# Performance work log

Hardware: AMD Instinct MI355X
Metric: run time of the kernel (lower is better)

The kernel has to match this reference:

```python
import jax, jax.numpy as jnp
import numpy as np

B, S, D = 4, 4096, 64
D_MODEL = 64


def setup_inputs() -> dict:
    key = jax.random.key(0)
    kq, kk, kv, km = jax.random.split(key, 4)
    q = jax.random.normal(kq, (B, S, D), dtype=jnp.float32)
    k = jax.random.normal(kk, (B, S, D), dtype=jnp.float32)
    v = jax.random.normal(kv, (B, S, D), dtype=jnp.float32)
    mask = jax.random.uniform(km, (B, S, S), dtype=jnp.float32)
    return {"q": q, "k": k, "v": v, "mask": mask}


def reference(q, k, v, mask):
    dk = jnp.sqrt(jnp.asarray(D_MODEL, dtype=q.dtype))
    # [B,S,S] scores; multiplicative (non-additive) mask applied pre-softmax
    scaled_qk = jnp.einsum('bqd,bkd->bqk', q, k) / dk
    scaled_qk = scaled_qk * mask
    attn = jax.nn.softmax(scaled_qk, axis=-1)
    return jnp.einsum('bqk,bkd->bqd', attn, v)
```

## Files before the change

kernel.cpp:

```cpp
#include <hip/hip_runtime.h>
#include <hip/hip_bf16.h>

#define S_LEN 4096
#define DH 64
#define NBATCH 4

typedef __attribute__((ext_vector_type(8))) short bf16x8;
typedef __attribute__((ext_vector_type(4))) short bf16x4;
typedef __attribute__((ext_vector_type(4))) float f32x4;

static __device__ __forceinline__ short f2bf(float x) {
  __hip_bfloat16 h = __float2bfloat16(x);
  return *reinterpret_cast<short*>(&h);
}

#define MFMA(a, b, c) __builtin_amdgcn_mfma_f32_16x16x32_bf16((a), (b), (c), 0, 0, 0)

__global__ __launch_bounds__(256) void cvt_q_kernel(const float* __restrict__ q,
                                                    short* __restrict__ qb) {
  int i = (blockIdx.x * 256 + threadIdx.x) * 4;
  f32x4 x = *(const f32x4*)(q + i);
  bf16x4 o;
#pragma unroll
  for (int j = 0; j < 4; ++j) o[j] = f2bf(x[j]);
  *(bf16x4*)(qb + i) = o;
}

__global__ __launch_bounds__(256) void cvt_frag_kernel(const float* __restrict__ k,
                                                       const float* __restrict__ v,
                                                       short* __restrict__ kfrag,
                                                       short* __restrict__ vfrag) {
  __shared__ short kt[32][80];
  __shared__ short vt[32][80];
  const int t = threadIdx.x;
  const int b = blockIdx.x >> 7;
  const int i = blockIdx.x & 127;
  const size_t src0 = ((size_t)b * S_LEN + i * 32) * DH;
  {
    const int row = t >> 3, c0 = (t & 7) * 8;
    const f32x4 xk0 = *(const f32x4*)(k + src0 + row * DH + c0);
    const f32x4 xk1 = *(const f32x4*)(k + src0 + row * DH + c0 + 4);
    const f32x4 xv0 = *(const f32x4*)(v + src0 + row * DH + c0);
    const f32x4 xv1 = *(const f32x4*)(v + src0 + row * DH + c0 + 4);
#pragma unroll
    for (int j = 0; j < 4; ++j) {
      kt[row][c0 + j] = f2bf(xk0[j]);  kt[row][c0 + 4 + j] = f2bf(xk1[j]);
      vt[row][c0 + j] = f2bf(xv0[j]);  vt[row][c0 + 4 + j] = f2bf(xv1[j]);
    }
  }
  __syncthreads();
  const int c = t >> 6, l = t & 63;
  const size_t dst = (((size_t)(b * 128 + i) * 4 + c) * 64 + l) * 8;
  {
    const int kr = ((c >> 1) * 16) + (l & 15);
    const int d0 = ((c & 1) * 32) + (l >> 4) * 8;
    *(bf16x8*)(kfrag + dst) = *(const bf16x8*)&kt[kr][d0];
  }
  {
    bf16x8 f;
    const int col = c * 16 + (l & 15);
    const int r0 = (l >> 4) * 8;
#pragma unroll
    for (int j = 0; j < 8; ++j) f[j] = vt[r0 + j][col];
    *(bf16x8*)(vfrag + dst) = f;
  }
}

__global__ __launch_bounds__(512, 2) void fa_kernel(
    const short* __restrict__ qb, const short* __restrict__ kfrag,
    const short* __restrict__ vfrag, const float* __restrict__ mask,
    float* __restrict__ out) {
  __shared__ __align__(16) short lds_p[8][16][40];
  __shared__ float lds_O[8][16][64];
  __shared__ float lds_l[8][16];

  const int tid = threadIdx.x;
  const int w = tid >> 6;
  const int wq = w >> 1;
  const int wk = w & 1;
  const int lane = tid & 63;
  const int quad = lane >> 4;
  const int n16 = lane & 15;
  const int loff = lane * 8;

  const int vb = ((blockIdx.x & 7) << 5) | (blockIdx.x >> 3);
  const int b = vb >> 6;
  const int q0 = (vb & 63) << 6;

  const int qr = q0 + wq * 16 + n16;
  const short* qrow = qb + (size_t)(b * S_LEN + qr) * DH;
  const bf16x8 aQ0 = *(const bf16x8*)(qrow + quad * 8);
  const bf16x8 aQ1 = *(const bf16x8*)(qrow + 32 + quad * 8);

  f32x4 O0 = {0.f, 0.f, 0.f, 0.f}, O1 = O0, O2 = O0, O3 = O0;
  float lacc = 0.f;

  const float* mrow = mask + ((size_t)b * S_LEN + qr) * S_LEN + quad * 4;
  const short* kfb = kfrag + (size_t)(b * 128 + wk) * 2048;
  const short* vfb = vfrag + (size_t)(b * 128 + wk) * 2048;

  bf16x8 kA0, kA1, kA2, kA3, kB0, kB1, kB2, kB3;
  bf16x8 vA0, vA1, vA2, vA3, vB0, vB1, vB2, vB3;
  f32x4 mA0, mA1, mB0, mB1, mC0, mC1, mD0, mD1;

#define LOAD_BK(B0, B1, B2, B3, SS)                       \
  {                                                       \
    const short* kf_ = kfb + (size_t)(SS) * 4096 + loff;  \
    B0 = *(const bf16x8*)(kf_);                           \
    B1 = *(const bf16x8*)(kf_ + 512);                     \
    B2 = *(const bf16x8*)(kf_ + 1024);                    \
    B3 = *(const bf16x8*)(kf_ + 1536);                    \
  }

#define LOAD_BV(V0, V1, V2, V3, SS)                       \
  {                                                       \
    const short* vf_ = vfb + (size_t)(SS) * 4096 + loff;  \
    V0 = *(const bf16x8*)(vf_);                           \
    V1 = *(const bf16x8*)(vf_ + 512);                     \
    V2 = *(const bf16x8*)(vf_ + 1024);                    \
    V3 = *(const bf16x8*)(vf_ + 1536);                    \
  }

#define LOAD_MASK(D0, D1, LK)                             \
  {                                                       \
    const float* mp_ = mrow + (LK);                       \
    D0 = *(const f32x4*)(mp_);                            \
    D1 = *(const f32x4*)(mp_ + 16);                       \
  }

#define FA_STEP(K0, K1, K2, K3, V0, V1, V2, V3, M0, M1, SS)                \
  {                                                                        \
    const f32x4 z = {0.f, 0.f, 0.f, 0.f};                                  \
    f32x4 s0 = MFMA(K0, aQ0, z); s0 = MFMA(K1, aQ1, s0);                   \
    f32x4 s1 = MFMA(K2, aQ0, z); s1 = MFMA(K3, aQ1, s1);                   \
    LOAD_BK(K0, K1, K2, K3, ((SS) + 2) & 63);          \
    float p0_[4], p1_[4];                                                  \
    _Pragma("unroll") for (int r = 0; r < 4; ++r) {                        \
      p0_[r] = __expf(s0[r] * 0.125f * M0[r]);                             \
      p1_[r] = __expf(s1[r] * 0.125f * M1[r]);                             \
      lacc += p0_[r] + p1_[r];                                             \
    }                                                                      \
    LOAD_MASK(M0, M1, (((SS) + 4) * 64 + wk * 32) & 4095);     \
    bf16x4 w0_, w1_;                                                       \
    _Pragma("unroll") for (int r = 0; r < 4; ++r) {                        \
      w0_[r] = f2bf(p0_[r]); w1_[r] = f2bf(p1_[r]);                        \
    }                                                                      \
    *(bf16x4*)&lds_p[w][n16][quad * 4] = w0_;                              \
    *(bf16x4*)&lds_p[w][n16][16 + quad * 4] = w1_;                         \
    const bf16x8 aP = *(const bf16x8*)&lds_p[w][n16][quad * 8];            \
    O0 = MFMA(aP, V0, O0); O1 = MFMA(aP, V1, O1);                          \
    O2 = MFMA(aP, V2, O2); O3 = MFMA(aP, V3, O3);                          \
    LOAD_BV(V0, V1, V2, V3, ((SS) + 2) & 63);          \
  }

  LOAD_BK(kA0, kA1, kA2, kA3, 0);
  LOAD_BK(kB0, kB1, kB2, kB3, 1);
  LOAD_BV(vA0, vA1, vA2, vA3, 0);
  LOAD_BV(vB0, vB1, vB2, vB3, 1);
  LOAD_MASK(mA0, mA1, wk * 32);
  LOAD_MASK(mB0, mB1, 64 + wk * 32);
  LOAD_MASK(mC0, mC1, 128 + wk * 32);
  LOAD_MASK(mD0, mD1, 192 + wk * 32);

#pragma unroll 1
  for (int it = 0; it < 16; ++it) {
    const int s4 = it * 4;
    FA_STEP(kA0, kA1, kA2, kA3, vA0, vA1, vA2, vA3, mA0, mA1, s4);
    FA_STEP(kB0, kB1, kB2, kB3, vB0, vB1, vB2, vB3, mB0, mB1, s4 + 1);
    FA_STEP(kA0, kA1, kA2, kA3, vA0, vA1, vA2, vA3, mC0, mC1, s4 + 2);
    FA_STEP(kB0, kB1, kB2, kB3, vB0, vB1, vB2, vB3, mD0, mD1, s4 + 3);
  }
#undef LOAD_BK
#undef LOAD_BV
#undef LOAD_MASK
#undef FA_STEP

  lacc += __shfl_xor(lacc, 16);
  lacc += __shfl_xor(lacc, 32);

#pragma unroll
  for (int r = 0; r < 4; ++r) {
    const int row = quad * 4 + r;
    lds_O[w][row][n16]      = O0[r];
    lds_O[w][row][16 + n16] = O1[r];
    lds_O[w][row][32 + n16] = O2[r];
    lds_O[w][row][48 + n16] = O3[r];
  }
  if (lane < 16) lds_l[w][lane] = lacc;
  __syncthreads();

  const int g = tid >> 7;
  const int r = (tid >> 3) & 15;
  const int c8 = (tid & 7) << 3;
  const int w0 = g * 2, w1 = g * 2 + 1;
  const float inv = 1.0f / (lds_l[w0][r] + lds_l[w1][r]);
  float* op = out + (size_t)(b * S_LEN + q0 + g * 16 + r) * DH + c8;
  f32x4 acc0, acc1;
#pragma unroll
  for (int j = 0; j < 4; ++j) {
    acc0[j] = (lds_O[w0][r][c8 + j]     + lds_O[w1][r][c8 + j])     * inv;
    acc1[j] = (lds_O[w0][r][c8 + 4 + j] + lds_O[w1][r][c8 + 4 + j]) * inv;
  }
  *(f32x4*)(op) = acc0;
  *(f32x4*)(op + 4) = acc1;
}

extern "C" void kernel_launch(void* const* d_in, const int* in_sizes, int n_in,
                              void* d_out, int out_size, void* d_ws, size_t ws_size,
                              hipStream_t stream) {
  const float* q = (const float*)d_in[0];
  const float* k = (const float*)d_in[1];
  const float* v = (const float*)d_in[2];
  const float* mask = (const float*)d_in[3];
  float* out = (float*)d_out;

  short* qb = (short*)d_ws;
  short* kfrag = qb + (size_t)NBATCH * S_LEN * DH;
  short* vfrag = kfrag + (size_t)NBATCH * S_LEN * DH;

  cvt_q_kernel<<<(NBATCH * S_LEN * DH) / 1024, 256, 0, stream>>>(q, qb);
  cvt_frag_kernel<<<NBATCH * 128, 256, 0, stream>>>(k, v, kfrag, vfrag);
  fa_kernel<<<NBATCH * 64, 512, 0, stream>>>(qb, kfrag, vfrag, mask, out);
}
```

Before: 402.9 us.

## Stage K/V fragments and mask tiles through double-buffered LDS

Replaces per-wave register prefetch of K/V fragments and mask values with cooperative loads by all 8 waves into double-buffered LDS, using XOR-swizzled mask slots. Each step reads the current tile from LDS and writes the next one, followed by a block-wide barrier. This removes the duplicate global loads of K/V made by waves that share the same key split, and shrinks register pressure. In exchange it adds a __syncthreads every step, LDS traffic, and a shorter prefetch distance (one step instead of two to four).

```diff
diff --git a/kernel.cpp b/kernel.cpp
--- a/kernel.cpp
+++ b/kernel.cpp
@@ -70,6 +70,9 @@
     const short* __restrict__ qb, const short* __restrict__ kfrag,
     const short* __restrict__ vfrag, const float* __restrict__ mask,
     float* __restrict__ out) {
+  __shared__ __align__(16) short kst[2][2][4][512];
+  __shared__ __align__(16) short vst[2][2][4][512];
+  __shared__ __align__(16) float mst[2][4096];
   __shared__ __align__(16) short lds_p[8][16][40];
   __shared__ float lds_O[8][16][64];
   __shared__ float lds_l[8][16];
@@ -95,52 +98,44 @@
   f32x4 O0 = {0.f, 0.f, 0.f, 0.f}, O1 = O0, O2 = O0, O3 = O0;
   float lacc = 0.f;
 
-  const float* mrow = mask + ((size_t)b * S_LEN + qr) * S_LEN + quad * 4;
-  const short* kfb = kfrag + (size_t)(b * 128 + wk) * 2048;
-  const short* vfb = vfrag + (size_t)(b * 128 + wk) * 2048;
-
-  bf16x8 kA0, kA1, kA2, kA3, kB0, kB1, kB2, kB3;
-  bf16x8 vA0, vA1, vA2, vA3, vB0, vB1, vB2, vB3;
-  f32x4 mA0, mA1, mB0, mB1, mC0, mC1, mD0, mD1;
-
-#define LOAD_BK(B0, B1, B2, B3, SS)                       \
-  {                                                       \
-    const short* kf_ = kfb + (size_t)(SS) * 4096 + loff;  \
-    B0 = *(const bf16x8*)(kf_);                           \
-    B1 = *(const bf16x8*)(kf_ + 512);                     \
-    B2 = *(const bf16x8*)(kf_ + 1024);                    \
-    B3 = *(const bf16x8*)(kf_ + 1536);                    \
-  }
-
-#define LOAD_BV(V0, V1, V2, V3, SS)                       \
-  {                                                       \
-    const short* vf_ = vfb + (size_t)(SS) * 4096 + loff;  \
-    V0 = *(const bf16x8*)(vf_);                           \
-    V1 = *(const bf16x8*)(vf_ + 512);                     \
-    V2 = *(const bf16x8*)(vf_ + 1024);                    \
-    V3 = *(const bf16x8*)(vf_ + 1536);                    \
-  }
-
-#define LOAD_MASK(D0, D1, LK)                             \
-  {                                                       \
-    const float* mp_ = mrow + (LK);                       \
-    D0 = *(const f32x4*)(mp_);                            \
-    D1 = *(const f32x4*)(mp_ + 16);                       \
-  }
-
-#define FA_STEP(K0, K1, K2, K3, V0, V1, V2, V3, M0, M1, SS)                \
+  const int ksp = w >> 2, kfr = w & 3;
+  const short* kbase =
+      kfrag + (size_t)(b * 128 + ksp) * 2048 + kfr * 512 + loff;
+  const short* vbase =
+      vfrag + (size_t)(b * 128 + ksp) * 2048 + kfr * 512 + loff;
+  const int srow0 = w * 8 + (lane >> 4);
+  const int srow1 = srow0 + 4;
+  const int sg = lane & 15;
+  const float* msrc0 =
+      mask + ((size_t)b * S_LEN + q0 + srow0) * S_LEN + sg * 4;
+  const float* msrc1 =
+      mask + ((size_t)b * S_LEN + q0 + srow1) * S_LEN + sg * 4;
+  const int wslot0 = srow0 * 64 + (sg ^ (srow0 & 7)) * 4;
+  const int wslot1 = srow1 * 64 + (sg ^ (srow1 & 7)) * 4;
+  const int mr = wq * 16 + n16;
+  const int rslot0 = mr * 64 + (((wk * 8 + quad) ^ (mr & 7)) * 4);
+  const int rslot1 = mr * 64 + (((wk * 8 + 4 + quad) ^ (mr & 7)) * 4);
+
+#define STEP(CUR, SS)                                                      \
   {                                                                        \
+    const int sn_ = ((SS) + 1) & 63; \
+    const bf16x8 kR = *(const bf16x8*)(kbase + (size_t)sn_ * 4096);        \
+    const bf16x8 vR = *(const bf16x8*)(vbase + (size_t)sn_ * 4096);        \
+    const f32x4 mR0 = *(const f32x4*)(msrc0 + sn_ * 64);                   \
+    const f32x4 mR1 = *(const f32x4*)(msrc1 + sn_ * 64);                   \
     const f32x4 z = {0.f, 0.f, 0.f, 0.f};                                  \
-    f32x4 s0 = MFMA(K0, aQ0, z); s0 = MFMA(K1, aQ1, s0);                   \
-    f32x4 s1 = MFMA(K2, aQ0, z); s1 = MFMA(K3, aQ1, s1);                   \
-    LOAD_BK(K0, K1, K2, K3, ((SS) + 2) & 63);          \
+    f32x4 s0 = MFMA(*(const bf16x8*)&kst[CUR][wk][0][loff], aQ0, z);       \
+    s0 = MFMA(*(const bf16x8*)&kst[CUR][wk][1][loff], aQ1, s0);            \
+    f32x4 s1 = MFMA(*(const bf16x8*)&kst[CUR][wk][2][loff], aQ0, z);       \
+    s1 = MFMA(*(const bf16x8*)&kst[CUR][wk][3][loff], aQ1, s1);            \
+    const f32x4 M0 = *(const f32x4*)&mst[CUR][rslot0];                     \
+    const f32x4 M1 = *(const f32x4*)&mst[CUR][rslot1];                     \
     float p0_[4], p1_[4];                                                  \
     _Pragma("unroll") for (int r = 0; r < 4; ++r) {                        \
       p0_[r] = __expf(s0[r] * 0.125f * M0[r]);                             \
       p1_[r] = __expf(s1[r] * 0.125f * M1[r]);                             \
       lacc += p0_[r] + p1_[r];                                             \
     }                                                                      \
-    LOAD_MASK(M0, M1, (((SS) + 4) * 64 + wk * 32) & 4095);     \
     bf16x4 w0_, w1_;                                                       \
     _Pragma("unroll") for (int r = 0; r < 4; ++r) {                        \
       w0_[r] = f2bf(p0_[r]); w1_[r] = f2bf(p1_[r]);                        \
@@ -148,32 +143,35 @@
     *(bf16x4*)&lds_p[w][n16][quad * 4] = w0_;                              \
     *(bf16x4*)&lds_p[w][n16][16 + quad * 4] = w1_;                         \
     const bf16x8 aP = *(const bf16x8*)&lds_p[w][n16][quad * 8];            \
-    O0 = MFMA(aP, V0, O0); O1 = MFMA(aP, V1, O1);                          \
-    O2 = MFMA(aP, V2, O2); O3 = MFMA(aP, V3, O3);                          \
-    LOAD_BV(V0, V1, V2, V3, ((SS) + 2) & 63);          \
-  }
-
-  LOAD_BK(kA0, kA1, kA2, kA3, 0);
-  LOAD_BK(kB0, kB1, kB2, kB3, 1);
-  LOAD_BV(vA0, vA1, vA2, vA3, 0);
-  LOAD_BV(vB0, vB1, vB2, vB3, 1);
-  LOAD_MASK(mA0, mA1, wk * 32);
-  LOAD_MASK(mB0, mB1, 64 + wk * 32);
-  LOAD_MASK(mC0, mC1, 128 + wk * 32);
-  LOAD_MASK(mD0, mD1, 192 + wk * 32);
+    O0 = MFMA(aP, *(const bf16x8*)&vst[CUR][wk][0][loff], O0);             \
+    O1 = MFMA(aP, *(const bf16x8*)&vst[CUR][wk][1][loff], O1);             \
+    O2 = MFMA(aP, *(const bf16x8*)&vst[CUR][wk][2][loff], O2);             \
+    O3 = MFMA(aP, *(const bf16x8*)&vst[CUR][wk][3][loff], O3);             \
+    *(bf16x8*)&kst[(CUR) ^ 1][ksp][kfr][loff] = kR;                        \
+    *(bf16x8*)&vst[(CUR) ^ 1][ksp][kfr][loff] = vR;                        \
+    *(f32x4*)&mst[(CUR) ^ 1][wslot0] = mR0;                                \
+    *(f32x4*)&mst[(CUR) ^ 1][wslot1] = mR1;                                \
+    __syncthreads();                                                       \
+  }
+
+  {
+    const bf16x8 kR = *(const bf16x8*)(kbase);
+    const bf16x8 vR = *(const bf16x8*)(vbase);
+    const f32x4 mR0 = *(const f32x4*)(msrc0);
+    const f32x4 mR1 = *(const f32x4*)(msrc1);
+    *(bf16x8*)&kst[0][ksp][kfr][loff] = kR;
+    *(bf16x8*)&vst[0][ksp][kfr][loff] = vR;
+    *(f32x4*)&mst[0][wslot0] = mR0;
+    *(f32x4*)&mst[0][wslot1] = mR1;
+    __syncthreads();
+  }
 
 #pragma unroll 1
-  for (int it = 0; it < 16; ++it) {
-    const int s4 = it * 4;
-    FA_STEP(kA0, kA1, kA2, kA3, vA0, vA1, vA2, vA3, mA0, mA1, s4);
-    FA_STEP(kB0, kB1, kB2, kB3, vB0, vB1, vB2, vB3, mB0, mB1, s4 + 1);
-    FA_STEP(kA0, kA1, kA2, kA3, vA0, vA1, vA2, vA3, mC0, mC1, s4 + 2);
-    FA_STEP(kB0, kB1, kB2, kB3, vB0, vB1, vB2, vB3, mD0, mD1, s4 + 3);
-  }
-#undef LOAD_BK
-#undef LOAD_BV
-#undef LOAD_MASK
-#undef FA_STEP
+  for (int it = 0; it < 32; ++it) {
+    STEP(0, 2 * it);
+    STEP(1, 2 * it + 1);
+  }
+#undef STEP
 
   lacc += __shfl_xor(lacc, 16);
   lacc += __shfl_xor(lacc, 32);
```

After: 393.4 us. 2.4% less time.

## Stage mask tiles into LDS via async global_load_lds double buffering

Applied to the files above, without the earlier changes.

Mask tiles are now loaded with asynchronous global-to-LDS copies into a double-buffered 128KB shared buffer, using XOR swizzling to avoid bank conflicts. Each wave reads its mask fragments from LDS instead of holding register-prefetched mask vectors, and a barrier with a vmcnt wait runs per 256-column stage. The change aims to make the dominant mask stream fully coalesced and to cut register pressure. It costs large LDS use that limits occupancy to about one block per CU, adds per-stage barriers, and the hand-counted vmcnt waits are fragile.

```diff
diff --git a/kernel.cpp b/kernel.cpp
--- a/kernel.cpp
+++ b/kernel.cpp
@@ -12,6 +12,12 @@
 static __device__ __forceinline__ short f2bf(float x) {
   __hip_bfloat16 h = __float2bfloat16(x);
   return *reinterpret_cast<short*>(&h);
+}
+
+static __device__ __forceinline__ void gl_lds16(const void* g, void* l) {
+  __builtin_amdgcn_global_load_lds(
+      (const __attribute__((address_space(1))) void*)g,
+      (__attribute__((address_space(3))) void*)l, 16, 0, 0);
 }
 
 #define MFMA(a, b, c) __builtin_amdgcn_mfma_f32_16x16x32_bf16((a), (b), (c), 0, 0, 0)
@@ -70,9 +76,8 @@
     const short* __restrict__ qb, const short* __restrict__ kfrag,
     const short* __restrict__ vfrag, const float* __restrict__ mask,
     float* __restrict__ out) {
+  __shared__ __align__(16) float mst[2][16384];
   __shared__ __align__(16) short lds_p[8][16][40];
-  __shared__ float lds_O[8][16][64];
-  __shared__ float lds_l[8][16];
 
   const int tid = threadIdx.x;
   const int w = tid >> 6;
@@ -95,13 +100,30 @@
   f32x4 O0 = {0.f, 0.f, 0.f, 0.f}, O1 = O0, O2 = O0, O3 = O0;
   float lacc = 0.f;
 
-  const float* mrow = mask + ((size_t)b * S_LEN + qr) * S_LEN + quad * 4;
   const short* kfb = kfrag + (size_t)(b * 128 + wk) * 2048;
   const short* vfb = vfrag + (size_t)(b * 128 + wk) * 2048;
-
   bf16x8 kA0, kA1, kA2, kA3, kB0, kB1, kB2, kB3;
   bf16x8 vA0, vA1, vA2, vA3, vB0, vB1, vB2, vB3;
-  f32x4 mA0, mA1, mB0, mB1, mC0, mC1, mD0, mD1;
+
+  const float* mbase =
+      mask + ((size_t)b * S_LEN + q0 + w * 8) * S_LEN;
+  const int mr = wq * 16 + n16;
+  const int mx = n16 & 7;
+  int rs0[4], rs1[4];
+#pragma unroll
+  for (int ssl = 0; ssl < 4; ++ssl) {
+    rs0[ssl] = mr * 256 + (((ssl * 16) + wk * 8 + quad) ^ mx) * 4;
+    rs1[ssl] = mr * 256 + (((ssl * 16) + wk * 8 + 4 + quad) ^ mx) * 4;
+  }
+
+#define STAGE(BUF, SS)                                                     \
+  {                                                                        \
+    const int c0_ = (SS) * 256;                                            \
+    _Pragma("unroll") for (int j = 0; j < 8; ++j) {                        \
+      gl_lds16(mbase + (size_t)j * S_LEN + c0_ + ((lane ^ j) << 2),        \
+               (char*)&mst[BUF][0] + (w * 8 + j) * 1024);                  \
+    }                                                                      \
+  }
 
 #define LOAD_BK(B0, B1, B2, B3, SS)                       \
   {                                                       \
@@ -121,26 +143,20 @@
     V3 = *(const bf16x8*)(vf_ + 1536);                    \
   }
 
-#define LOAD_MASK(D0, D1, LK)                             \
-  {                                                       \
-    const float* mp_ = mrow + (LK);                       \
-    D0 = *(const f32x4*)(mp_);                            \
-    D1 = *(const f32x4*)(mp_ + 16);                       \
-  }
-
-#define FA_STEP(K0, K1, K2, K3, V0, V1, V2, V3, M0, M1, SS)                \
+#define SUB(K0, K1, K2, K3, V0, V1, V2, V3, MB, SSL, GS)                   \
   {                                                                        \
     const f32x4 z = {0.f, 0.f, 0.f, 0.f};                                  \
     f32x4 s0 = MFMA(K0, aQ0, z); s0 = MFMA(K1, aQ1, s0);                   \
     f32x4 s1 = MFMA(K2, aQ0, z); s1 = MFMA(K3, aQ1, s1);                   \
-    LOAD_BK(K0, K1, K2, K3, ((SS) + 2) & 63);          \
+    LOAD_BK(K0, K1, K2, K3, ((GS) + 2) & 63);          \
+    const f32x4 M0 = *(const f32x4*)((MB) + rs0[SSL]);                     \
+    const f32x4 M1 = *(const f32x4*)((MB) + rs1[SSL]);                     \
     float p0_[4], p1_[4];                                                  \
     _Pragma("unroll") for (int r = 0; r < 4; ++r) {                        \
       p0_[r] = __expf(s0[r] * 0.125f * M0[r]);                             \
       p1_[r] = __expf(s1[r] * 0.125f * M1[r]);                             \
       lacc += p0_[r] + p1_[r];                                             \
     }                                                                      \
-    LOAD_MASK(M0, M1, (((SS) + 4) * 64 + wk * 32) & 4095);     \
     bf16x4 w0_, w1_;                                                       \
     _Pragma("unroll") for (int r = 0; r < 4; ++r) {                        \
       w0_[r] = f2bf(p0_[r]); w1_[r] = f2bf(p1_[r]);                        \
@@ -150,30 +166,38 @@
     const bf16x8 aP = *(const bf16x8*)&lds_p[w][n16][quad * 8];            \
     O0 = MFMA(aP, V0, O0); O1 = MFMA(aP, V1, O1);                          \
     O2 = MFMA(aP, V2, O2); O3 = MFMA(aP, V3, O3);                          \
-    LOAD_BV(V0, V1, V2, V3, ((SS) + 2) & 63);          \
-  }
-
+    LOAD_BV(V0, V1, V2, V3, ((GS) + 2) & 63);          \
+  }
+
+  STAGE(0, 0);
   LOAD_BK(kA0, kA1, kA2, kA3, 0);
+  LOAD_BV(vA0, vA1, vA2, vA3, 0);
   LOAD_BK(kB0, kB1, kB2, kB3, 1);
-  LOAD_BV(vA0, vA1, vA2, vA3, 0);
   LOAD_BV(vB0, vB1, vB2, vB3, 1);
-  LOAD_MASK(mA0, mA1, wk * 32);
-  LOAD_MASK(mB0, mB1, 64 + wk * 32);
-  LOAD_MASK(mC0, mC1, 128 + wk * 32);
-  LOAD_MASK(mD0, mD1, 192 + wk * 32);
-
+  asm volatile("s_waitcnt vmcnt(16)\n\ts_barrier" ::: "memory");
+
+  int buf = 0;
 #pragma unroll 1
-  for (int it = 0; it < 16; ++it) {
-    const int s4 = it * 4;
-    FA_STEP(kA0, kA1, kA2, kA3, vA0, vA1, vA2, vA3, mA0, mA1, s4);
-    FA_STEP(kB0, kB1, kB2, kB3, vB0, vB1, vB2, vB3, mB0, mB1, s4 + 1);
-    FA_STEP(kA0, kA1, kA2, kA3, vA0, vA1, vA2, vA3, mC0, mC1, s4 + 2);
-    FA_STEP(kB0, kB1, kB2, kB3, vB0, vB1, vB2, vB3, mD0, mD1, s4 + 3);
-  }
+  for (int s = 0; s < 16; ++s) {
+    STAGE(buf ^ 1, (s + 1) & 15);
+    const float* mb = &mst[buf][0];
+    const int gs = s * 4;
+    SUB(kA0, kA1, kA2, kA3, vA0, vA1, vA2, vA3, mb, 0, gs);
+    SUB(kB0, kB1, kB2, kB3, vB0, vB1, vB2, vB3, mb, 1, gs + 1);
+    SUB(kA0, kA1, kA2, kA3, vA0, vA1, vA2, vA3, mb, 2, gs + 2);
+    SUB(kB0, kB1, kB2, kB3, vB0, vB1, vB2, vB3, mb, 3, gs + 3);
+    asm volatile("s_waitcnt vmcnt(16)\n\ts_barrier" ::: "memory");
+    buf ^= 1;
+  }
+#undef STAGE
 #undef LOAD_BK
 #undef LOAD_BV
-#undef LOAD_MASK
-#undef FA_STEP
+#undef SUB
+
+  asm volatile("s_waitcnt vmcnt(0)\n\ts_barrier" ::: "memory");
+
+  float* ldsO = &mst[0][0];
+  float* ldsl = &mst[1][0];
 
   lacc += __shfl_xor(lacc, 16);
   lacc += __shfl_xor(lacc, 32);
@@ -181,25 +205,28 @@
 #pragma unroll
   for (int r = 0; r < 4; ++r) {
     const int row = quad * 4 + r;
-    lds_O[w][row][n16]      = O0[r];
-    lds_O[w][row][16 + n16] = O1[r];
-    lds_O[w][row][32 + n16] = O2[r];
-    lds_O[w][row][48 + n16] = O3[r];
-  }
-  if (lane < 16) lds_l[w][lane] = lacc;
+    float* od = ldsO + (w * 16 + row) * 64;
+    od[n16]      = O0[r];
+    od[16 + n16] = O1[r];
+    od[32 + n16] = O2[r];
+    od[48 + n16] = O3[r];
+  }
+  if (lane < 16) ldsl[w * 16 + lane] = lacc;
   __syncthreads();
 
   const int g = tid >> 7;
-  const int r = (tid >> 3) & 15;
+  const int rr = (tid >> 3) & 15;
   const int c8 = (tid & 7) << 3;
-  const int w0 = g * 2, w1 = g * 2 + 1;
-  const float inv = 1.0f / (lds_l[w0][r] + lds_l[w1][r]);
-  float* op = out + (size_t)(b * S_LEN + q0 + g * 16 + r) * DH + c8;
+  const int wa = g * 2, wb = g * 2 + 1;
+  const float inv = 1.0f / (ldsl[wa * 16 + rr] + ldsl[wb * 16 + rr]);
+  const float* oap = ldsO + (wa * 16 + rr) * 64 + c8;
+  const float* obp = ldsO + (wb * 16 + rr) * 64 + c8;
+  float* op = out + (size_t)(b * S_LEN + q0 + g * 16 + rr) * DH + c8;
   f32x4 acc0, acc1;
 #pragma unroll
   for (int j = 0; j < 4; ++j) {
-    acc0[j] = (lds_O[w0][r][c8 + j]     + lds_O[w1][r][c8 + j])     * inv;
-    acc1[j] = (lds_O[w0][r][c8 + 4 + j] + lds_O[w1][r][c8 + 4 + j]) * inv;
+    acc0[j] = (oap[j]     + obp[j])     * inv;
+    acc1[j] = (oap[4 + j] + obp[4 + j]) * inv;
   }
   *(f32x4*)(op) = acc0;
   *(f32x4*)(op + 4) = acc1;
```

New measurement: 388.6 us. -3.5%, faster.
